# Optimization experiments

Measured on AMD Instinct MI355X. Metric: run time of the kernel, lower is better.

The kernel has to match this reference:

```python
import jax, jax.numpy as jnp
import numpy as np

B, N, D = 4, 160, 64
ZI, ZE, L, LE = 64, 64, 4, 8
H1, H2 = 128, 64


def setup_inputs() -> dict:
    key = jax.random.key(0)
    ks = jax.random.split(key, 20)
    s = 0.05
    inp = {
        "node_embeddings": jax.random.normal(ks[0], (B, N, D), jnp.float32),
        "z_intra_t": jax.random.normal(ks[1], (B, ZI), jnp.float32),
        "z_inter_t": jax.random.normal(ks[2], (B, ZE), jnp.float32),
        # lag embedding table
        "lag_emb": jax.random.normal(ks[3], (L, LE), jnp.float32),
        # instantaneous reasoner: (2D+ZI)->128->64->1
        "Wi1": jax.random.normal(ks[4], (2 * D + ZI, H1), jnp.float32) * s,
        "bi1": jnp.zeros((H1,), jnp.float32),
        "Wi2": jax.random.normal(ks[5], (H1, H2), jnp.float32) * s,
        "bi2": jnp.zeros((H2,), jnp.float32),
        "Wi3": jax.random.normal(ks[6], (H2, 1), jnp.float32) * s,
        "bi3": jnp.zeros((1,), jnp.float32),
        # lagged reasoner: (2D+ZE+LE)->128->64->1
        "Wl1": jax.random.normal(ks[7], (2 * D + ZE + LE, H1), jnp.float32) * s,
        "bl1": jnp.zeros((H1,), jnp.float32),
        "Wl2": jax.random.normal(ks[8], (H1, H2), jnp.float32) * s,
        "bl2": jnp.zeros((H2,), jnp.float32),
        "Wl3": jax.random.normal(ks[9], (H2, 1), jnp.float32) * s,
        "bl3": jnp.zeros((1,), jnp.float32),
    }
    return inp


def reference(node_embeddings, z_intra_t, z_inter_t, lag_emb,
              Wi1, bi1, Wi2, bi2, Wi3, bi3,
              Wl1, bl1, Wl2, bl2, Wl3, bl3):
    # Instead of materializing concat([h_i, h_j, z, ...]) over N*N pairs,
    # split the first linear layer's weight along its input rows; the sum of
    # per-part projections equals the linear over the concatenation.
    ne = node_embeddings  # [B, N, D]

    # --- instantaneous reasoner ---
    Wi1_a, Wi1_b, Wi1_z = Wi1[:D], Wi1[D:2 * D], Wi1[2 * D:]
    pi = ne @ Wi1_a          # [B, N, H1] projection of h_i
    pj = ne @ Wi1_b          # [B, N, H1] projection of h_j
    pz = z_intra_t @ Wi1_z   # [B, H1]
    h = jax.nn.relu(pi[:, :, None, :] + pj[:, None, :, :]
                    + pz[:, None, None, :] + bi1)          # [B, N, N, H1]
    h = jax.nn.relu(h @ Wi2 + bi2)                         # [B, N, N, H2]
    W_logits = (h @ Wi3 + bi3)[..., 0]                     # [B, N, N]

    # --- lagged reasoner ---
    Wl1_a, Wl1_b = Wl1[:D], Wl1[D:2 * D]
    Wl1_z, Wl1_l = Wl1[2 * D:2 * D + ZE], Wl1[2 * D + ZE:]
    qi = ne @ Wl1_a          # [B, N, H1]
    qj = ne @ Wl1_b          # [B, N, H1]
    qz = z_inter_t @ Wl1_z   # [B, H1]
    ql = lag_emb @ Wl1_l     # [L, H1]
    g = jax.nn.relu(qi[:, None, :, None, :] + qj[:, None, None, :, :]
                    + qz[:, None, None, None, :] + ql[None, :, None, None, :]
                    + bl1)                                 # [B, L, N, N, H1]
    g = jax.nn.relu(g @ Wl2 + bl2)                         # [B, L, N, N, H2]
    A_logits = (g @ Wl3 + bl3)[..., 0]                     # [B, L, N, N]

    mask = 1.0 - jnp.eye(N, dtype=ne.dtype)
    W_t = jax.nn.sigmoid(W_logits) * mask
    A_lags_t = jax.nn.sigmoid(A_logits) * mask
    return (W_t, A_lags_t)
```

## Files before the change

kernel.cpp:

```cpp
#include <hip/hip_runtime.h>
#include <hip/hip_bf16.h>

#define B_   4
#define N_   160
#define D_   64
#define ZI_  64
#define H1_  128
#define H2_  64
#define L_   4
#define LE_  8

typedef __bf16 bf16x8 __attribute__((ext_vector_type(8)));
typedef float  f32x4  __attribute__((ext_vector_type(4)));

__global__ __launch_bounds__(128) void stage_a(
    const float* __restrict__ ne,
    const float* __restrict__ zi,
    const float* __restrict__ ze,
    const float* __restrict__ lag,
    const float* __restrict__ Wi1,
    const float* __restrict__ bi1,
    const float* __restrict__ Wl1,
    const float* __restrict__ bl1,
    float* __restrict__ ui, float* __restrict__ uq,
    __bf16* __restrict__ vpi, __bf16* __restrict__ vpl)
{
    const int bi = blockIdx.x;
    const int b  = bi / N_;
    const int h  = threadIdx.x;

    const float* nerow = ne + bi * D_;

    float pi_ = 0.f, pj_ = 0.f, qi_ = 0.f, qj_ = 0.f;
#pragma unroll 16
    for (int d = 0; d < D_; ++d) {
        const float a = nerow[d];
        pi_ += a * Wi1[d * H1_ + h];
        pj_ += a * Wi1[(D_ + d) * H1_ + h];
        qi_ += a * Wl1[d * H1_ + h];
        qj_ += a * Wl1[(D_ + d) * H1_ + h];
    }
    float pz = 0.f, qz = 0.f;
#pragma unroll 16
    for (int z = 0; z < ZI_; ++z) {
        pz += zi[b * ZI_ + z] * Wi1[(2 * D_ + z) * H1_ + h];
        qz += ze[b * ZI_ + z] * Wl1[(2 * D_ + z) * H1_ + h];
    }

    ui[bi * H1_ + h]  = pi_ + pz + bi1[h];
    vpi[bi * H1_ + h] = (__bf16)pj_;
    vpl[bi * H1_ + h] = (__bf16)qj_;

    const float qbase = qi_ + qz + bl1[h];
#pragma unroll
    for (int l = 0; l < L_; ++l) {
        float ql = 0.f;
#pragma unroll
        for (int e = 0; e < LE_; ++e)
            ql += lag[l * LE_ + e] * Wl1[(2 * D_ + ZI_ + e) * H1_ + h];
        uq[((b * L_ + l) * N_ + (bi % N_)) * H1_ + h] = qbase + ql;
    }
}

__global__ __launch_bounds__(256) void stage_b(
    const float* __restrict__ ui, const float* __restrict__ uq,
    const __bf16* __restrict__ vpi, const __bf16* __restrict__ vpl,
    const float* __restrict__ Wi2, const float* __restrict__ bi2,
    const float* __restrict__ Wi3, const float* __restrict__ bi3,
    const float* __restrict__ Wl2, const float* __restrict__ bl2,
    const float* __restrict__ Wl3, const float* __restrict__ bl3,
    float* __restrict__ out)
{
    __shared__ __bf16 panel[N_ * H1_];

    const int t    = threadIdx.x;
    const int wid  = t >> 6;
    const int lane = t & 63;
    const int q = lane >> 4;
    const int c = lane & 15;

    const int blk  = blockIdx.x;
    const int wave = blk * 4 + wid;

    const __bf16* psrc;
    if (blk < 160) psrc = vpi + (blk / 40) * (N_ * H1_);
    else           psrc = vpl + ((blk - 160) / 160) * (N_ * H1_);

    const float* ubase;
    const float *W2, *b2, *w3;
    float b3f;
    long  obase;
    int   i;
    if (wave < B_ * N_) {
        i = wave % N_;
        ubase = ui + wave * H1_;
        W2 = Wi2; b2 = bi2; w3 = Wi3; b3f = bi3[0];
        obase = (long)wave * N_;
    } else {
        const int w2i = wave - B_ * N_;
        i = w2i % N_;
        ubase = uq + w2i * H1_;
        W2 = Wl2; b2 = bl2; w3 = Wl3; b3f = bl3[0];
        obase = (long)B_ * N_ * N_ + (long)w2i * N_;
    }

    bf16x8 stg[10];
#pragma unroll
    for (int it = 0; it < 10; ++it)
        stg[it] = *(const bf16x8*)(psrc + 2048 * it + 8 * t);

    bf16x8 bfr[4][4];
#pragma unroll
    for (int kt = 0; kt < 4; ++kt)
#pragma unroll
        for (int ct = 0; ct < 4; ++ct) {
            bf16x8 tt;
#pragma unroll
            for (int j = 0; j < 8; ++j)
                tt[j] = (__bf16)W2[(32 * kt + 8 * q + j) * H2_ + 16 * ct + c];
            bfr[kt][ct] = tt;
        }

    f32x4 u0[4], u1[4];
#pragma unroll
    for (int kt = 0; kt < 4; ++kt) {
        const float* up = ubase + 32 * kt + 8 * q;
        u0[kt] = *(const f32x4*)(up);
        u1[kt] = *(const f32x4*)(up + 4);
    }

    float b2c[4], w3c[4];
#pragma unroll
    for (int ct = 0; ct < 4; ++ct) {
        b2c[ct] = b2[16 * ct + c];
        w3c[ct] = w3[16 * ct + c];
    }

    {
        const int gsw = (t & 15) ^ ((t >> 4) & 7);
        const int rowbase = (t >> 4) * H1_ + gsw * 8;
#pragma unroll
        for (int it = 0; it < 10; ++it)
            *(bf16x8*)(panel + 16 * it * H1_ + rowbase) = stg[it];
    }
    __syncthreads();

    for (int jt = 0; jt < 10; ++jt) {
        const __bf16* prow = panel + (16 * jt + c) * H1_;
        f32x4 acc[4];
#pragma unroll
        for (int ct = 0; ct < 4; ++ct) acc[ct] = (f32x4)0.0f;

#pragma unroll
        for (int kt = 0; kt < 4; ++kt) {
            const bf16x8 vb = *(const bf16x8*)(prow + (((4 * kt + q) ^ (c & 7)) << 3));
            bf16x8 a;
#pragma unroll
            for (int j = 0; j < 4; ++j) {
                a[j]     = (__bf16)fmaxf(u0[kt][j] + (float)vb[j],     0.f);
                a[4 + j] = (__bf16)fmaxf(u1[kt][j] + (float)vb[4 + j], 0.f);
            }
#pragma unroll
            for (int ct = 0; ct < 4; ++ct)
                acc[ct] = __builtin_amdgcn_mfma_f32_16x16x32_bf16(
                    a, bfr[kt][ct], acc[ct], 0, 0, 0);
        }

        float logit[4];
#pragma unroll
        for (int r = 0; r < 4; ++r) {
            float p = 0.f;
#pragma unroll
            for (int ct = 0; ct < 4; ++ct) {
                const float h2 = fmaxf(acc[ct][r] + b2c[ct], 0.f);
                p += h2 * w3c[ct];
            }
            p += __shfl_xor(p, 1);
            p += __shfl_xor(p, 2);
            p += __shfl_xor(p, 4);
            p += __shfl_xor(p, 8);
            logit[r] = p;
        }

        if (c < 4) {
            const int j = 16 * jt + 4 * q + c;
            const float lg = logit[c] + b3f;
            const float s = (j == i) ? 0.f : 1.f / (1.f + __expf(-lg));
            out[obase + j] = s;
        }
    }
}

extern "C" void kernel_launch(void* const* d_in, const int* in_sizes, int n_in,
                              void* d_out, int out_size, void* d_ws, size_t ws_size,
                              hipStream_t stream) {
    const float* ne  = (const float*)d_in[0];
    const float* zi  = (const float*)d_in[1];
    const float* ze  = (const float*)d_in[2];
    const float* lag = (const float*)d_in[3];
    const float* Wi1 = (const float*)d_in[4];
    const float* bi1 = (const float*)d_in[5];
    const float* Wi2 = (const float*)d_in[6];
    const float* bi2 = (const float*)d_in[7];
    const float* Wi3 = (const float*)d_in[8];
    const float* bi3 = (const float*)d_in[9];
    const float* Wl1 = (const float*)d_in[10];
    const float* bl1 = (const float*)d_in[11];
    const float* Wl2 = (const float*)d_in[12];
    const float* bl2 = (const float*)d_in[13];
    const float* Wl3 = (const float*)d_in[14];
    const float* bl3 = (const float*)d_in[15];

    float*  ws  = (float*)d_ws;
    float*  ui  = ws;
    float*  uqw = ws + 81920;
    __bf16* vpi = (__bf16*)(ws + 409600);
    __bf16* vpl = vpi + 81920;

    stage_a<<<B_ * N_, 128, 0, stream>>>(ne, zi, ze, lag, Wi1, bi1, Wl1, bl1,
                                         ui, uqw, vpi, vpl);

    stage_b<<<(B_ * N_ + B_ * L_ * N_) / 4, 256, 0, stream>>>(
        ui, uqw, vpi, vpl,
        Wi2, bi2, Wi3, bi3, Wl2, bl2, Wl3, bl3,
        (float*)d_out);
}
```

Baseline: 116.8 us.

## Rewrite stage_a projection as bf16 MFMA tiles and fold bias into accumulator

The first-layer projection kernel now handles 16-row tiles per block, with four waves computing the i/j projections for both reasoners through bf16 MFMA. The concatenated [ne, z] input is processed as a single K=128 MFMA, replacing the per-thread scalar FMA loops over 640 blocks. The grid shrinks from 640 blocks to 40. Stage_b now preloads the layer-2 bias into the accumulator and unrolls its j-tile loop by two. The trade-offs are that ne, z and the first-layer weights are rounded to bf16, which adds precision loss to ui/uq, and that stage_a runs on only 40 blocks, so it may underuse the GPU.

New measurement: 122.3 us. +4.7%, slower.

```diff
diff --git a/kernel.cpp b/kernel.cpp
--- a/kernel.cpp
+++ b/kernel.cpp
@@ -13,7 +13,7 @@
 typedef __bf16 bf16x8 __attribute__((ext_vector_type(8)));
 typedef float  f32x4  __attribute__((ext_vector_type(4)));
 
-__global__ __launch_bounds__(128) void stage_a(
+__global__ __launch_bounds__(256, 1) void stage_a(
     const float* __restrict__ ne,
     const float* __restrict__ zi,
     const float* __restrict__ ze,
@@ -25,40 +25,100 @@
     float* __restrict__ ui, float* __restrict__ uq,
     __bf16* __restrict__ vpi, __bf16* __restrict__ vpl)
 {
-    const int bi = blockIdx.x;
-    const int b  = bi / N_;
-    const int h  = threadIdx.x;
-
-    const float* nerow = ne + bi * D_;
-
-    float pi_ = 0.f, pj_ = 0.f, qi_ = 0.f, qj_ = 0.f;
-#pragma unroll 16
-    for (int d = 0; d < D_; ++d) {
-        const float a = nerow[d];
-        pi_ += a * Wi1[d * H1_ + h];
-        pj_ += a * Wi1[(D_ + d) * H1_ + h];
-        qi_ += a * Wl1[d * H1_ + h];
-        qj_ += a * Wl1[(D_ + d) * H1_ + h];
-    }
-    float pz = 0.f, qz = 0.f;
-#pragma unroll 16
-    for (int z = 0; z < ZI_; ++z) {
-        pz += zi[b * ZI_ + z] * Wi1[(2 * D_ + z) * H1_ + h];
-        qz += ze[b * ZI_ + z] * Wl1[(2 * D_ + z) * H1_ + h];
-    }
-
-    ui[bi * H1_ + h]  = pi_ + pz + bi1[h];
-    vpi[bi * H1_ + h] = (__bf16)pj_;
-    vpl[bi * H1_ + h] = (__bf16)qj_;
-
-    const float qbase = qi_ + qz + bl1[h];
-#pragma unroll
-    for (int l = 0; l < L_; ++l) {
-        float ql = 0.f;
-#pragma unroll
-        for (int e = 0; e < LE_; ++e)
-            ql += lag[l * LE_ + e] * Wl1[(2 * D_ + ZI_ + e) * H1_ + h];
-        uq[((b * L_ + l) * N_ + (bi % N_)) * H1_ + h] = qbase + ql;
+    const int mt   = blockIdx.x;
+    const int w    = threadIdx.x >> 6;
+    const int lane = threadIdx.x & 63;
+    const int q = lane >> 4;
+    const int c = lane & 15;
+
+    const int r0 = mt * 16;
+    const int b  = mt / 10;
+    const int i0 = r0 - b * N_;
+
+    const float* W1   = (w < 2) ? Wi1 : Wl1;
+    const bool   colb = (w & 1);
+    const float* zv   = (w == 2) ? (ze + b * ZI_) : (zi + b * ZI_);
+    const int    nkt  = colb ? 2 : 4;
+
+    bf16x8 af[4];
+#pragma unroll
+    for (int kt = 0; kt < 2; ++kt) {
+        const float* ap = ne + (r0 + c) * D_ + 32 * kt + 8 * q;
+        const f32x4 x0 = *(const f32x4*)ap;
+        const f32x4 x1 = *(const f32x4*)(ap + 4);
+        bf16x8 t;
+#pragma unroll
+        for (int j = 0; j < 4; ++j) { t[j] = (__bf16)x0[j]; t[4 + j] = (__bf16)x1[j]; }
+        af[kt] = t;
+    }
+    if (!colb) {
+#pragma unroll
+        for (int kt = 2; kt < 4; ++kt) {
+            const float* ap = zv + 32 * (kt - 2) + 8 * q;
+            const f32x4 x0 = *(const f32x4*)ap;
+            const f32x4 x1 = *(const f32x4*)(ap + 4);
+            bf16x8 t;
+#pragma unroll
+            for (int j = 0; j < 4; ++j) { t[j] = (__bf16)x0[j]; t[4 + j] = (__bf16)x1[j]; }
+            af[kt] = t;
+        }
+    }
+
+#pragma unroll
+    for (int nt = 0; nt < 8; ++nt) {
+        const int col = 16 * nt + c;
+
+        bf16x8 bfr[4];
+#pragma unroll
+        for (int kt = 0; kt < 4; ++kt) {
+            if (kt >= nkt) break;
+            bf16x8 t;
+#pragma unroll
+            for (int j = 0; j < 8; ++j) {
+                const int k = 32 * kt + 8 * q + j;
+                const int wrow = (colb || kt >= 2) ? (64 + k) : k;
+                t[j] = (__bf16)W1[wrow * H1_ + col];
+            }
+            bfr[kt] = t;
+        }
+
+        float binit = 0.f;
+        if (w == 0) binit = bi1[col];
+        if (w == 2) binit = bl1[col];
+        f32x4 acc = {binit, binit, binit, binit};
+
+#pragma unroll
+        for (int kt = 0; kt < 4; ++kt) {
+            if (kt >= nkt) break;
+            acc = __builtin_amdgcn_mfma_f32_16x16x32_bf16(af[kt], bfr[kt], acc, 0, 0, 0);
+        }
+
+        if (w == 0) {
+#pragma unroll
+            for (int rr = 0; rr < 4; ++rr)
+                ui[(r0 + 4 * q + rr) * H1_ + col] = acc[rr];
+        } else if (w == 1) {
+#pragma unroll
+            for (int rr = 0; rr < 4; ++rr)
+                vpi[(r0 + 4 * q + rr) * H1_ + col] = (__bf16)acc[rr];
+        } else if (w == 3) {
+#pragma unroll
+            for (int rr = 0; rr < 4; ++rr)
+                vpl[(r0 + 4 * q + rr) * H1_ + col] = (__bf16)acc[rr];
+        } else {
+            float lw[4] = {0.f, 0.f, 0.f, 0.f};
+#pragma unroll
+            for (int e = 0; e < LE_; ++e) {
+                const float we = Wl1[(2 * D_ + ZI_ + e) * H1_ + col];
+#pragma unroll
+                for (int l = 0; l < L_; ++l) lw[l] += lag[l * LE_ + e] * we;
+            }
+#pragma unroll
+            for (int l = 0; l < L_; ++l)
+#pragma unroll
+                for (int rr = 0; rr < 4; ++rr)
+                    uq[((b * L_ + l) * N_ + i0 + 4 * q + rr) * H1_ + col] = acc[rr] + lw[l];
+        }
     }
 }
 
@@ -145,11 +205,13 @@
     }
     __syncthreads();
 
+#pragma unroll 2
     for (int jt = 0; jt < 10; ++jt) {
         const __bf16* prow = panel + (16 * jt + c) * H1_;
         f32x4 acc[4];
 #pragma unroll
-        for (int ct = 0; ct < 4; ++ct) acc[ct] = (f32x4)0.0f;
+        for (int ct = 0; ct < 4; ++ct)
+            acc[ct] = (f32x4){b2c[ct], b2c[ct], b2c[ct], b2c[ct]};
 
 #pragma unroll
         for (int kt = 0; kt < 4; ++kt) {
@@ -172,7 +234,7 @@
             float p = 0.f;
 #pragma unroll
             for (int ct = 0; ct < 4; ++ct) {
-                const float h2 = fmaxf(acc[ct][r] + b2c[ct], 0.f);
+                const float h2 = fmaxf(acc[ct][r], 0.f);
                 p += h2 * w3c[ct];
             }
             p += __shfl_xor(p, 1);
@@ -217,8 +279,8 @@
     __bf16* vpi = (__bf16*)(ws + 409600);
     __bf16* vpl = vpi + 81920;
 
-    stage_a<<<B_ * N_, 128, 0, stream>>>(ne, zi, ze, lag, Wi1, bi1, Wl1, bl1,
-                                         ui, uqw, vpi, vpl);
+    stage_a<<<40, 256, 0, stream>>>(ne, zi, ze, lag, Wi1, bi1, Wl1, bl1,
+                                    ui, uqw, vpi, vpl);
 
     stage_b<<<(B_ * N_ + B_ * L_ * N_) / 4, 256, 0, stream>>>(
         ui, uqw, vpi, vpl,
```
